# Optimization experiments

Hardware: AMD Instinct MI355X
Metric: run time of the kernel (lower is better)

Reference implementation:

```python
import jax, jax.numpy as jnp
import numpy as np


def _lstm_last(x, w_ih, w_hh, b_ih, b_hh):
    # x: [M, T, D] -> last hidden state [M, H]; PyTorch gate order i,f,g,o
    M = x.shape[0]
    H = w_hh.shape[1]
    xi = jnp.einsum('mtd,gd->tmg', x, w_ih) + b_ih + b_hh  # [T, M, 4H]
    def step(carry, xt):
        h, c = carry
        gates = xt + h @ w_hh.T
        i, f, g, o = jnp.split(gates, 4, axis=-1)
        c = jax.nn.sigmoid(f) * c + jax.nn.sigmoid(i) * jnp.tanh(g)
        h = jax.nn.sigmoid(o) * jnp.tanh(c)
        return (h, c), None
    z = jnp.zeros((M, H), x.dtype)
    (h, _), _ = jax.lax.scan(step, (z, z), xi)
    return h


def _gcn_conv(x, edge_index, w, b):
    # Symmetric-normalized GCN conv with self loops (PyG GCNConv defaults).
    # x: [BT, N, F] -> [BT, N, Hg]
    N = x.shape[1]
    loops = jnp.arange(N, dtype=edge_index.dtype)
    src = jnp.concatenate([edge_index[0], loops])
    dst = jnp.concatenate([edge_index[1], loops])
    deg = jnp.zeros((N,), x.dtype).at[dst].add(jnp.ones((), x.dtype))
    dinv = jax.lax.rsqrt(deg)  # deg >= 1 thanks to self loops
    norm = (dinv[src] * dinv[dst])[:, None]  # [E+N, 1]
    xw = x @ w                               # [BT, N, Hg]
    msg = xw[:, src, :] * norm               # gather along node axis
    out = jnp.zeros_like(xw).at[:, dst, :].add(msg)  # scatter-add
    return out + b


def setup_inputs() -> dict:
    key = jax.random.key(0)
    ks = jax.random.split(key, 16)
    B, T, N, F = 2, 12, 10000, 16
    Hg, H, P, E = 32, 64, 4, 160000
    sc = 0.1
    return {
        'era5_seq': jax.random.normal(ks[0], (B, T, N, F), jnp.float32),
        'zeta_seq': jax.random.normal(ks[1], (B, T, N), jnp.float32),
        'edge_index': jax.random.randint(ks[2], (2, E), 0, N, jnp.int32),
        'gcn_w': jax.random.normal(ks[3], (F, Hg), jnp.float32) * sc,
        'gcn_b': jnp.zeros((Hg,), jnp.float32),
        'w_ih1': jax.random.normal(ks[4], (4 * H, Hg), jnp.float32) * sc,
        'w_hh1': jax.random.normal(ks[5], (4 * H, H), jnp.float32) * sc,
        'b_ih1': jax.random.normal(ks[6], (4 * H,), jnp.float32) * sc,
        'b_hh1': jax.random.normal(ks[7], (4 * H,), jnp.float32) * sc,
        'w_ih2': jax.random.normal(ks[8], (4 * H, 1), jnp.float32) * sc,
        'w_hh2': jax.random.normal(ks[9], (4 * H, H), jnp.float32) * sc,
        'b_ih2': jax.random.normal(ks[10], (4 * H,), jnp.float32) * sc,
        'b_hh2': jax.random.normal(ks[11], (4 * H,), jnp.float32) * sc,
        'fc_w': jax.random.normal(ks[12], (P, 2 * H), jnp.float32) * sc,
        'fc_b': jnp.zeros((P,), jnp.float32),
    }


def reference(era5_seq, zeta_seq, edge_index, gcn_w, gcn_b, w_ih1, w_hh1, b_ih1, b_hh1, w_ih2, w_hh2, b_ih2, b_hh2, fc_w, fc_b):
    B, T, N, F = era5_seq.shape
    Hg = gcn_w.shape[1]
    # GCN over all (b, t) slices at once (replaces nested python loops)
    h = _gcn_conv(era5_seq.reshape(B * T, N, F), edge_index, gcn_w, gcn_b)
    gcn_seq = h.reshape(B, T, N, Hg).transpose(0, 2, 1, 3).reshape(B * N, T, Hg)
    spatial_feat = _lstm_last(gcn_seq, w_ih1, w_hh1, b_ih1, b_hh1)  # [B*N, H]
    z_seq = zeta_seq.transpose(0, 2, 1).reshape(B * N, T, 1)
    zeta_feat = _lstm_last(z_seq, w_ih2, w_hh2, b_ih2, b_hh2)        # [B*N, H]
    combined = jnp.concatenate([spatial_feat, zeta_feat], axis=-1)
    y = combined @ fc_w.T + fc_b                                     # [B*N, P]
    return y.reshape(B, N, -1).transpose(0, 2, 1)                    # [B, P, N]
```

## Files before the change

### kernel.cpp

```cpp
#include <hip/hip_runtime.h>
#include <hip/hip_bf16.h>
#include <stdint.h>

#define NN 10000
#define EE 160000
#define BB 2
#define TT 12
#define FF 16
#define HG 32
#define HH 64
#define PP 4
#define BT (BB*TT)
#define MM (BB*NN)
#define CAP 96
#define L2E 1.4426950408889634f

typedef _Float16 half8 __attribute__((ext_vector_type(8)));
typedef _Float16 h2 __attribute__((ext_vector_type(2)));
typedef float f32x4 __attribute__((ext_vector_type(4)));

union UP { uint32_t u; h2 h; };

__device__ __forceinline__ float sigm2(float a) {
  return __builtin_amdgcn_rcpf(1.0f + __builtin_amdgcn_exp2f(-a));
}
__device__ __forceinline__ float tanh2(float a) {
  return fmaf(-2.0f, __builtin_amdgcn_rcpf(1.0f + __builtin_amdgcn_exp2f(a)), 1.0f);
}

#define FILL_BLKS (EE / 256)
#define PREP_BLKS ((NN * BT * 8) / 256)
__global__ __launch_bounds__(256) void k_prepfill(
    const int* __restrict__ eidx, int* __restrict__ cnt, int* __restrict__ csr,
    const float* __restrict__ era5, uint32_t* __restrict__ xt) {
  const int bid = blockIdx.x;
  if (bid < FILL_BLKS) {
    int e = bid * 256 + threadIdx.x;
    int d = eidx[EE + e];
    int pos = atomicAdd(&cnt[d], 1);
    if (pos < CAP) csr[d * CAP + pos] = eidx[e];
  } else {
    int D = (bid - FILL_BLKS) * 256 + threadIdx.x;
    int f2 = D & 7;
    int bt = (D >> 3) % BT;
    int n = D / (8 * BT);
    const float* src = era5 + ((size_t)bt * NN + n) * FF + f2 * 2;
    UP u; u.h[0] = (_Float16)src[0]; u.h[1] = (_Float16)src[1];
    xt[D] = u.u;
  }
}

__global__ __launch_bounds__(256) void k_gather(const uint32_t* __restrict__ xt,
                                                const int* __restrict__ csr,
                                                const int* __restrict__ cnt,
                                                const float* __restrict__ gw,
                                                const float* __restrict__ gb,
                                                uint32_t* __restrict__ gout) {
  __shared__ float wsm[FF * HG];
  __shared__ float gbs[HG];
  __shared__ float agg[4][BT][FF];
  const int tid = threadIdx.x;
  wsm[tid] = gw[tid];
  wsm[tid + 256] = gw[tid + 256];
  if (tid < HG) gbs[tid] = gb[tid];

  const int dloc = tid >> 6, lane = tid & 63;
  const int dst = blockIdx.x * 4 + dloc;
  const int cdst = min(cnt[dst], CAP);
  const float dinv_d = rsqrtf((float)cdst + 1.0f);

  float acc[6];
#pragma unroll
  for (int i = 0; i < 6; ++i) acc[i] = 0.f;

  for (int base = 0; base < cdst; base += 64) {
    int mine = base + lane;
    int sv = dst; float dvv = 0.f;
    if (mine < cdst) {
      sv = csr[dst * CAP + mine];
      dvv = rsqrtf((float)cnt[sv] + 1.0f);
    }
    const int lim = min(64, cdst - base);
    for (int j = 0; j < lim; j += 4) {
      int sj[4]; float dj[4];
#pragma unroll
      for (int u = 0; u < 4; ++u) {
        int idx = j + u;
        sj[u] = __shfl(sv, idx);
        float d = __shfl(dvv, idx);
        dj[u] = (idx < lim) ? d : 0.f;
      }
      uint32_t dw[4][3];
#pragma unroll
      for (int u = 0; u < 4; ++u) {
        const uint32_t* row = xt + (size_t)sj[u] * 192;
#pragma unroll
        for (int k = 0; k < 3; ++k) dw[u][k] = row[lane + 64 * k];
      }
#pragma unroll
      for (int u = 0; u < 4; ++u) {
#pragma unroll
        for (int k = 0; k < 3; ++k) {
          UP up; up.u = dw[u][k];
          acc[2 * k]     = fmaf((float)up.h[0], dj[u], acc[2 * k]);
          acc[2 * k + 1] = fmaf((float)up.h[1], dj[u], acc[2 * k + 1]);
        }
      }
    }
  }
  const uint32_t* srow = xt + (size_t)dst * 192;
#pragma unroll
  for (int k = 0; k < 3; ++k) {
    UP u; u.u = srow[lane + 64 * k];
    int d0 = lane + 64 * k;
    int bt = d0 >> 3, f = (d0 & 7) * 2;
    agg[dloc][bt][f]     = (acc[2 * k]     + (float)u.h[0] * dinv_d) * dinv_d;
    agg[dloc][bt][f + 1] = (acc[2 * k + 1] + (float)u.h[1] * dinv_d) * dinv_d;
  }
  __syncthreads();
#pragma unroll
  for (int k = 0; k < 3; ++k) {
    int d0 = lane + 64 * k;
    int t = d0 >> 4, c0 = (d0 & 15) * 2;
#pragma unroll
    for (int b = 0; b < 2; ++b) {
      const float* av = agg[dloc][b * TT + t];
      float v0 = gbs[c0], v1 = gbs[c0 + 1];
#pragma unroll
      for (int f = 0; f < FF; ++f) {
        v0 = fmaf(av[f], wsm[f * HG + c0], v0);
        v1 = fmaf(av[f], wsm[f * HG + c0 + 1], v1);
      }
      UP u; u.h[0] = (_Float16)v0; u.h[1] = (_Float16)v1;
      gout[((size_t)(b * NN + dst)) * 192 + d0] = u.u;
    }
  }
}

__global__ __launch_bounds__(256) void k_lstmfc(
    const _Float16* __restrict__ gout, const float* __restrict__ zeta,
    const float* __restrict__ w_ih1, const float* __restrict__ w_hh1,
    const float* __restrict__ b_ih1, const float* __restrict__ b_hh1,
    const float* __restrict__ w_ih2, const float* __restrict__ w_hh2,
    const float* __restrict__ b_ih2, const float* __restrict__ b_hh2,
    const float* __restrict__ fc_w, const float* __restrict__ fc_b,
    float* __restrict__ out) {
  const int m0 = blockIdx.x * 16;
  const int b = (m0 >= NN) ? 1 : 0;
  const int n0 = m0 - b * NN;
  const int tid = threadIdx.x;
  const int wave = tid >> 6;
  const int lane = tid & 63;
  const int col = lane & 15;
  const int quad = lane >> 4;

  half8 Bx[4];
  half8 Bh1[4][2];
  half8 Bh2[4][2];
  float bias1[4], bias2[4], wx[4];
#pragma unroll
  for (int g = 0; g < 4; ++g) {
    const float sc = (g == 2) ? 2.0f * L2E : L2E;
    int ncol = 16 * (wave + 4 * g) + col;
    bias1[g] = (b_ih1[ncol] + b_hh1[ncol]) * sc;
    bias2[g] = (b_ih2[ncol] + b_hh2[ncol]) * sc;
    wx[g] = w_ih2[ncol] * sc;
#pragma unroll
    for (int j = 0; j < 8; ++j)
      Bx[g][j] = (_Float16)(w_ih1[ncol * HG + quad * 8 + j] * sc);
#pragma unroll
    for (int c2 = 0; c2 < 2; ++c2) {
#pragma unroll
      for (int j = 0; j < 8; ++j) {
        Bh1[g][c2][j] = (_Float16)(w_hh1[ncol * HH + c2 * 32 + quad * 8 + j] * sc);
        Bh2[g][c2][j] = (_Float16)(w_hh2[ncol * HH + c2 * 32 + quad * 8 + j] * sc);
      }
    }
  }

  __shared__ float zbuf[TT][16];
  if (tid < TT * 16) {
    int t = tid >> 4, s = tid & 15;
    zbuf[t][s] = zeta[((size_t)b * TT + t) * NN + n0 + s];
  }
  __shared__ __align__(16) _Float16 hb1[2][16 * 72];
  __shared__ __align__(16) _Float16 hb2[2][16 * 72];
  __shared__ float fcb[16][132];

  const _Float16* gbase = gout + (size_t)(m0 + col) * (TT * HG) + quad * 8;
  half8 A0 = *(const half8*)(gbase);

  float c1[4] = {0.f, 0.f, 0.f, 0.f}, c2v[4] = {0.f, 0.f, 0.f, 0.f};
  float h1f[4], h2f[4];

  __syncthreads();

#pragma unroll
  for (int t = 0; t < TT; ++t) {
    const int p = t & 1;
    if (t > 0) {
#pragma unroll
      for (int r = 0; r < 4; ++r) {
        int a = (quad * 4 + r) * 72 + 16 * wave + col;
        hb1[p][a] = (_Float16)h1f[r];
        hb2[p][a] = (_Float16)h2f[r];
      }
    }
    f32x4 a1[4], a2[4];
#pragma unroll
    for (int g = 0; g < 4; ++g) {
      f32x4 ai; ai[0] = bias1[g]; ai[1] = bias1[g]; ai[2] = bias1[g]; ai[3] = bias1[g];
      a1[g] = __builtin_amdgcn_mfma_f32_16x16x32_f16(A0, Bx[g], ai, 0, 0, 0);
#pragma unroll
      for (int r = 0; r < 4; ++r)
        a2[g][r] = fmaf(wx[g], zbuf[t][quad * 4 + r], bias2[g]);
    }
    if (t < TT - 1) A0 = *(const half8*)(gbase + (t + 1) * HG);
    if (t > 0) {
      __syncthreads();
      const half8 A11 = *(const half8*)(&hb1[p][col * 72 + quad * 8]);
      const half8 A21 = *(const half8*)(&hb1[p][col * 72 + 32 + quad * 8]);
      const half8 A12 = *(const half8*)(&hb2[p][col * 72 + quad * 8]);
      const half8 A22 = *(const half8*)(&hb2[p][col * 72 + 32 + quad * 8]);
#pragma unroll
      for (int g = 0; g < 4; ++g) {
        a1[g] = __builtin_amdgcn_mfma_f32_16x16x32_f16(A11, Bh1[g][0], a1[g], 0, 0, 0);
        a1[g] = __builtin_amdgcn_mfma_f32_16x16x32_f16(A21, Bh1[g][1], a1[g], 0, 0, 0);
        a2[g] = __builtin_amdgcn_mfma_f32_16x16x32_f16(A12, Bh2[g][0], a2[g], 0, 0, 0);
        a2[g] = __builtin_amdgcn_mfma_f32_16x16x32_f16(A22, Bh2[g][1], a2[g], 0, 0, 0);
      }
    }
#pragma unroll
    for (int r = 0; r < 4; ++r) {
      float i1 = sigm2(a1[0][r]), f1 = sigm2(a1[1][r]);
      float g1 = tanh2(a1[2][r]), o1 = sigm2(a1[3][r]);
      c1[r] = fmaf(f1, c1[r], i1 * g1);
      h1f[r] = o1 * tanh2(c1[r] * (2.0f * L2E));
      float i2 = sigm2(a2[0][r]), f2 = sigm2(a2[1][r]);
      float g2 = tanh2(a2[2][r]), o2 = sigm2(a2[3][r]);
      c2v[r] = fmaf(f2, c2v[r], i2 * g2);
      h2f[r] = o2 * tanh2(c2v[r] * (2.0f * L2E));
    }
  }
#pragma unroll
  for (int r = 0; r < 4; ++r) {
    fcb[quad * 4 + r][16 * wave + col] = h1f[r];
    fcb[quad * 4 + r][64 + 16 * wave + col] = h2f[r];
  }
  __syncthreads();
  if (tid < 64) {
    int pp = tid >> 4, s = tid & 15;
    const f32x4* wr = (const f32x4*)(fc_w + pp * 128);
    const float* hv = fcb[s];
    float acc = fc_b[pp];
#pragma unroll
    for (int k = 0; k < 32; ++k) {
      f32x4 w4 = wr[k];
      acc += w4[0] * hv[4 * k] + w4[1] * hv[4 * k + 1] +
             w4[2] * hv[4 * k + 2] + w4[3] * hv[4 * k + 3];
    }
    out[((size_t)(b * PP + pp)) * NN + n0 + s] = acc;
  }
}

extern "C" void kernel_launch(void* const* d_in, const int* in_sizes, int n_in,
                              void* d_out, int out_size, void* d_ws, size_t ws_size,
                              hipStream_t stream) {
  (void)in_sizes; (void)n_in; (void)out_size; (void)ws_size;
  const float* era5  = (const float*)d_in[0];
  const float* zeta  = (const float*)d_in[1];
  const int*   eidx  = (const int*)d_in[2];
  const float* gcn_w = (const float*)d_in[3];
  const float* gcn_b = (const float*)d_in[4];
  const float* w_ih1 = (const float*)d_in[5];
  const float* w_hh1 = (const float*)d_in[6];
  const float* b_ih1 = (const float*)d_in[7];
  const float* b_hh1 = (const float*)d_in[8];
  const float* w_ih2 = (const float*)d_in[9];
  const float* w_hh2 = (const float*)d_in[10];
  const float* b_ih2 = (const float*)d_in[11];
  const float* b_hh2 = (const float*)d_in[12];
  const float* fc_w  = (const float*)d_in[13];
  const float* fc_b  = (const float*)d_in[14];
  float* out = (float*)d_out;

  char* ws = (char*)d_ws;
  int*      cnt  = (int*)(ws);
  int*      csr  = (int*)(ws + (64 << 10));
  uint32_t* xt   = (uint32_t*)(ws + (4ull << 20));
  _Float16* gout = (_Float16*)(ws + (12ull << 20));

  hipMemsetAsync(cnt, 0, NN * sizeof(int), stream);
  k_prepfill<<<FILL_BLKS + PREP_BLKS, 256, 0, stream>>>(eidx, cnt, csr, era5, xt);
  k_gather<<<NN / 4, 256, 0, stream>>>(xt, csr, cnt, gcn_w, gcn_b, (uint32_t*)gout);
  k_lstmfc<<<MM / 16, 256, 0, stream>>>(gout, zeta, w_ih1, w_hh1, b_ih1, b_hh1,
                                        w_ih2, w_hh2, b_ih2, b_hh2, fc_w, fc_b, out);
}
```

Before: 182.4 us.

## Split GCN gather per batch half across waves and raise LSTM occupancy

```diff
diff --git a/kernel.cpp b/kernel.cpp
--- a/kernel.cpp
+++ b/kernel.cpp
@@ -39,15 +39,15 @@
     int d = eidx[EE + e];
     int pos = atomicAdd(&cnt[d], 1);
     if (pos < CAP) csr[d * CAP + pos] = eidx[e];
-  } else {
-    int D = (bid - FILL_BLKS) * 256 + threadIdx.x;
-    int f2 = D & 7;
-    int bt = (D >> 3) % BT;
-    int n = D / (8 * BT);
-    const float* src = era5 + ((size_t)bt * NN + n) * FF + f2 * 2;
-    UP u; u.h[0] = (_Float16)src[0]; u.h[1] = (_Float16)src[1];
-    xt[D] = u.u;
-  }
+    return;
+  }
+  int D = (bid - FILL_BLKS) * 256 + threadIdx.x;
+  int f2 = D & 7;
+  int bt = (D >> 3) % BT;
+  int n = D / (8 * BT);
+  const float* src = era5 + ((size_t)bt * NN + n) * FF + f2 * 2;
+  UP u; u.h[0] = (_Float16)src[0]; u.h[1] = (_Float16)src[1];
+  xt[D] = u.u;
 }
 
 __global__ __launch_bounds__(256) void k_gather(const uint32_t* __restrict__ xt,
@@ -58,20 +58,19 @@
                                                 uint32_t* __restrict__ gout) {
   __shared__ float wsm[FF * HG];
   __shared__ float gbs[HG];
-  __shared__ float agg[4][BT][FF];
+  __shared__ float agg[4][192];
   const int tid = threadIdx.x;
   wsm[tid] = gw[tid];
   wsm[tid + 256] = gw[tid + 256];
   if (tid < HG) gbs[tid] = gb[tid];
 
-  const int dloc = tid >> 6, lane = tid & 63;
-  const int dst = blockIdx.x * 4 + dloc;
+  const int wave = tid >> 6, lane = tid & 63;
+  const int g = blockIdx.x * 4 + wave;
+  const int dst = g >> 1, bh = g & 1;
   const int cdst = min(cnt[dst], CAP);
   const float dinv_d = rsqrtf((float)cdst + 1.0f);
 
-  float acc[6];
-#pragma unroll
-  for (int i = 0; i < 6; ++i) acc[i] = 0.f;
+  float a0 = 0.f, a1 = 0.f, a2 = 0.f, a3 = 0.f;
 
   for (int base = 0; base < cdst; base += 64) {
     int mine = base + lane;
@@ -81,63 +80,63 @@
       dvv = rsqrtf((float)cnt[sv] + 1.0f);
     }
     const int lim = min(64, cdst - base);
-    for (int j = 0; j < lim; j += 4) {
-      int sj[4]; float dj[4];
-#pragma unroll
-      for (int u = 0; u < 4; ++u) {
+    for (int j = 0; j < lim; j += 8) {
+      int sj[8]; float dj[8];
+#pragma unroll
+      for (int u = 0; u < 8; ++u) {
         int idx = j + u;
         sj[u] = __shfl(sv, idx);
         float d = __shfl(dvv, idx);
         dj[u] = (idx < lim) ? d : 0.f;
       }
-      uint32_t dw[4][3];
-#pragma unroll
-      for (int u = 0; u < 4; ++u) {
-        const uint32_t* row = xt + (size_t)sj[u] * 192;
-#pragma unroll
-        for (int k = 0; k < 3; ++k) dw[u][k] = row[lane + 64 * k];
-      }
-#pragma unroll
-      for (int u = 0; u < 4; ++u) {
-#pragma unroll
-        for (int k = 0; k < 3; ++k) {
-          UP up; up.u = dw[u][k];
-          acc[2 * k]     = fmaf((float)up.h[0], dj[u], acc[2 * k]);
-          acc[2 * k + 1] = fmaf((float)up.h[1], dj[u], acc[2 * k + 1]);
-        }
-      }
-    }
-  }
-  const uint32_t* srow = xt + (size_t)dst * 192;
+      uint32_t dw0[8], dw1[8];
+#pragma unroll
+      for (int u = 0; u < 8; ++u) {
+        const uint32_t* row = xt + (size_t)sj[u] * 192 + bh * 96;
+        dw0[u] = row[lane];
+        dw1[u] = (lane < 32) ? row[64 + lane] : 0u;
+      }
+#pragma unroll
+      for (int u = 0; u < 8; ++u) {
+        UP p0; p0.u = dw0[u];
+        a0 = fmaf((float)p0.h[0], dj[u], a0);
+        a1 = fmaf((float)p0.h[1], dj[u], a1);
+        UP p1; p1.u = dw1[u];
+        a2 = fmaf((float)p1.h[0], dj[u], a2);
+        a3 = fmaf((float)p1.h[1], dj[u], a3);
+      }
+    }
+  }
+  const uint32_t* srow = xt + (size_t)dst * 192 + bh * 96;
+  {
+    UP s0; s0.u = srow[lane];
+    agg[wave][2 * lane]     = (a0 + (float)s0.h[0] * dinv_d) * dinv_d;
+    agg[wave][2 * lane + 1] = (a1 + (float)s0.h[1] * dinv_d) * dinv_d;
+    if (lane < 32) {
+      UP s1; s1.u = srow[64 + lane];
+      agg[wave][128 + 2 * lane] = (a2 + (float)s1.h[0] * dinv_d) * dinv_d;
+      agg[wave][129 + 2 * lane] = (a3 + (float)s1.h[1] * dinv_d) * dinv_d;
+    }
+  }
+  __syncthreads();
 #pragma unroll
   for (int k = 0; k < 3; ++k) {
-    UP u; u.u = srow[lane + 64 * k];
-    int d0 = lane + 64 * k;
-    int bt = d0 >> 3, f = (d0 & 7) * 2;
-    agg[dloc][bt][f]     = (acc[2 * k]     + (float)u.h[0] * dinv_d) * dinv_d;
-    agg[dloc][bt][f + 1] = (acc[2 * k + 1] + (float)u.h[1] * dinv_d) * dinv_d;
-  }
-  __syncthreads();
-#pragma unroll
-  for (int k = 0; k < 3; ++k) {
-    int d0 = lane + 64 * k;
-    int t = d0 >> 4, c0 = (d0 & 15) * 2;
-#pragma unroll
-    for (int b = 0; b < 2; ++b) {
-      const float* av = agg[dloc][b * TT + t];
-      float v0 = gbs[c0], v1 = gbs[c0 + 1];
-#pragma unroll
-      for (int f = 0; f < FF; ++f) {
-        v0 = fmaf(av[f], wsm[f * HG + c0], v0);
-        v1 = fmaf(av[f], wsm[f * HG + c0 + 1], v1);
-      }
-      UP u; u.h[0] = (_Float16)v0; u.h[1] = (_Float16)v1;
-      gout[((size_t)(b * NN + dst)) * 192 + d0] = u.u;
-    }
-  }
-}
-
-__global__ __launch_bounds__(256) void k_lstmfc(
+    int d0 = 64 * k + lane;
+    int t = d0 >> 4;
+    int c0 = (d0 & 15) * 2;
+    const float* av = &agg[wave][t * 16];
+    float v0 = gbs[c0], v1 = gbs[c0 + 1];
+#pragma unroll
+    for (int f = 0; f < FF; ++f) {
+      v0 = fmaf(av[f], wsm[f * HG + c0], v0);
+      v1 = fmaf(av[f], wsm[f * HG + c0 + 1], v1);
+    }
+    UP u; u.h[0] = (_Float16)v0; u.h[1] = (_Float16)v1;
+    gout[((size_t)(bh * NN + dst)) * 192 + d0] = u.u;
+  }
+}
+
+__global__ __launch_bounds__(256, 5) void k_lstmfc(
     const _Float16* __restrict__ gout, const float* __restrict__ zeta,
     const float* __restrict__ w_ih1, const float* __restrict__ w_hh1,
     const float* __restrict__ b_ih1, const float* __restrict__ b_hh1,
@@ -292,7 +291,8 @@
 
   hipMemsetAsync(cnt, 0, NN * sizeof(int), stream);
   k_prepfill<<<FILL_BLKS + PREP_BLKS, 256, 0, stream>>>(eidx, cnt, csr, era5, xt);
-  k_gather<<<NN / 4, 256, 0, stream>>>(xt, csr, cnt, gcn_w, gcn_b, (uint32_t*)gout);
+  k_gather<<<(2 * NN) / 4, 256, 0, stream>>>(xt, csr, cnt, gcn_w, gcn_b,
+                                             (uint32_t*)gout);
   k_lstmfc<<<MM / 16, 256, 0, stream>>>(gout, zeta, w_ih1, w_hh1, b_ih1, b_hh1,
                                         w_ih2, w_hh2, b_ih2, b_hh2, fc_w, fc_b, out);
 }
```

Result: slower. 393.5 us (+115.8%).
